# Kernel tuning notes

Hardware: AMD Instinct MI355X
Metric: run time of the kernel (lower is better)

## Reference

```python
import jax, jax.numpy as jnp
import numpy as np

B, QUE, VAL, D = 4, 128, 128, 512

def setup_inputs() -> dict:
    key = jax.random.key(0)
    k = jax.random.split(key, 8)
    return {
        "qs_1": jax.random.normal(k[0], (B, QUE, D), jnp.float32),
        "qs_2": jax.random.normal(k[1], (B, QUE, D), jnp.float32),  # unused by forward, kept for signature fidelity
        "ks":   jax.random.normal(k[2], (B, VAL, D), jnp.float32),
        "vs":   jax.random.normal(k[3], (B, VAL, D), jnp.float32),
        "sg_mask": jax.random.randint(k[4], (B, VAL), 0, 2).astype(bool),  # True = masked
        "W1":  jax.random.normal(k[5], (D, D), jnp.float32) / np.sqrt(D),
        "b1":  jnp.zeros((D,), jnp.float32),
        "Wse": jax.random.normal(k[6], (D, D), jnp.float32) / np.sqrt(D),
        "bse": jnp.zeros((D,), jnp.float32),
        "W2":  jax.random.normal(k[7], (D, 1), jnp.float32) / np.sqrt(D),
        "b2":  jnp.zeros((1,), jnp.float32),
    }

def reference(qs_1, qs_2, ks, vs, sg_mask, W1, b1, Wse, bse, W2, b2):
    # Pairwise query-key elementwise product: [B, que, val, d]
    x = qs_1[:, :, None, :] * ks[:, None, :, :]
    # linear1: Linear(d,d) + ReLU (dropout = identity at eval)
    h = jax.nn.relu(jnp.einsum('bqvd,de->bqve', x, W1) + b1)
    # linear2: Linear(d,1) + ReLU -> scalar score per (q, v) pair
    s = jax.nn.relu(jnp.einsum('bqvd,do->bqvo', h, W2) + b2)[..., 0]  # [B, que, val]
    m = sg_mask[:, None, :]                      # [B, 1, val], True = masked out
    # masked mean of h over the val axis (masked_fill(0) then divide by valid count)
    h = jnp.where(m[..., None], 0.0, h)
    denom = jnp.sum(~sg_mask, axis=-1).astype(h.dtype)      # [B]
    mean = h.sum(axis=2) / denom[:, None, None]             # [B, que, d]
    # squeeze-excitation gate: sigmoid(relu(Linear(d,d)))
    gate = jax.nn.sigmoid(jax.nn.relu(mean @ Wse + bse))    # [B, que, d]
    # masked softmax over val, weighted sum of values
    s = jnp.where(m, -1e9, s)
    w = jax.nn.softmax(s, axis=-1)                          # [B, que, val]
    out = jnp.einsum('bqv,bvd->bqd', w, vs)                 # [B, que, d]
    return gate * out
```

## Files before the change

kernel.cpp:

```cpp
#include <hip/hip_runtime.h>
#include <stdint.h>
#include <stddef.h>

#define BDIM 4
#define QUE  128
#define VAL  128
#define DD   512
#define BQ   (BDIM*QUE)
#define BK   32
#define SROW(r) ((((r) + ((r) >> 2))) & 3)

typedef float    f32x4 __attribute__((ext_vector_type(4)));
typedef float    f32x2 __attribute__((ext_vector_type(2)));
typedef _Float16 f16x8 __attribute__((ext_vector_type(8)));
typedef _Float16 f16x4 __attribute__((ext_vector_type(4)));
typedef _Float16 f16x2 __attribute__((ext_vector_type(2)));

typedef const __attribute__((address_space(1))) void* gas_ptr;
typedef __attribute__((address_space(3))) void*       las_ptr;

__device__ __forceinline__ void async_copy16(const void* g, void* l) {
    __builtin_amdgcn_global_load_lds((gas_ptr)g, (las_ptr)l, 16, 0, 0);
}

__global__ __launch_bounds__(256) void prep_kernel(const float* __restrict__ W1,
                                                   _Float16* __restrict__ W1T,
                                                   const float* __restrict__ Wse,
                                                   _Float16* __restrict__ WseT,
                                                   const float* __restrict__ vs,
                                                   _Float16* __restrict__ vsT) {
    __shared__ float tile[32][33];
    const int tx = threadIdx.x & 31;
    const int ty = threadIdx.x >> 5;
    const int gx = blockIdx.x, gy = blockIdx.y;
    if (gy < 32) {
        const float* src = (gy < 16) ? W1  : Wse;
        _Float16*    dst = (gy < 16) ? W1T : WseT;
        int a0 = gx * 32;
        int b0 = (gy & 15) * 32;
        #pragma unroll
        for (int r = 0; r < 4; ++r)
            tile[ty + r*8][tx] = src[(size_t)(a0 + ty + r*8) * DD + b0 + tx];
        __syncthreads();
        #pragma unroll
        for (int r = 0; r < 4; ++r) {
            int el = ty + r*8;
            dst[(size_t)(b0 + el) * DD + a0 + tx] = (_Float16)tile[tx][el];
        }
    } else {
        int bb = gy - 32;
        const float* src = vs  + (size_t)bb * VAL * DD;
        _Float16*    dst = vsT + (size_t)bb * DD * VAL;
        int b0 = gx * 32;
        for (int vt = 0; vt < 4; ++vt) {
            int a0 = vt * 32;
            __syncthreads();
            #pragma unroll
            for (int r = 0; r < 4; ++r)
                tile[ty + r*8][tx] = src[(size_t)(a0 + ty + r*8) * DD + b0 + tx];
            __syncthreads();
            #pragma unroll
            for (int r = 0; r < 4; ++r) {
                int el = ty + r*8;
                dst[(size_t)(b0 + el) * VAL + a0 + tx] = (_Float16)tile[tx][el];
            }
        }
    }
}

__global__ __launch_bounds__(512, 4) void gemm_h_kernel(
    const float* __restrict__ qs1,
    const float* __restrict__ ks,
    const int*   __restrict__ sgmask,
    const _Float16* __restrict__ W1T,
    const float* __restrict__ b1,
    const float* __restrict__ W2,
    float* __restrict__ s_part,
    float* __restrict__ meansum)
{
    __shared__ _Float16 Ah[128 * BK];
    __shared__ _Float16 Bh[256 * BK];
    __shared__ float qrow[DD];
    __shared__ float sred[4][VAL];
    __shared__ float msumLDS[2][256];

    const int tid  = threadIdx.x;
    const int bq   = blockIdx.x;
    const int gy   = blockIdx.y;
    const int b    = bq >> 7;
    const int lane = tid & 63;
    const int wid  = tid >> 6;
    const int wm   = wid >> 2;
    const int wn   = wid & 3;
    const int quad = lane >> 4;
    const int lr   = lane & 15;

    if (tid < 128)
        *(f32x4*)(qrow + tid * 4) = *(const f32x4*)(qs1 + (size_t)bq * DD + tid * 4);

    f32x4 acc[4][4];
    #pragma unroll
    for (int i = 0; i < 4; ++i)
        #pragma unroll
        for (int j = 0; j < 4; ++j) acc[i][j] = (f32x4){0.f, 0.f, 0.f, 0.f};

    const int r4 = tid >> 2;
    const int cs = tid & 3;
    const int ca = (cs - SROW(r4)) & 3;
    const float* ksrow = ks + ((size_t)b * VAL + r4) * DD + ca * 8;
    const float* qbase = qrow + ca * 8;
    _Float16* a_dst = &Ah[r4 * BK + cs * 8];
    const int rb1 = 128 + r4;
    const int cb1 = (cs - SROW(rb1)) & 3;
    const _Float16* gB0 = W1T + (size_t)(gy * 256 + r4) * DD + ca * 8;
    const _Float16* gB1 = W1T + (size_t)(gy * 256 + rb1) * DD + cb1 * 8;
    _Float16* ldsB0 = &Bh[(wid * 16) * BK];
    _Float16* ldsB1 = &Bh[(128 + wid * 16) * BK];

    const _Float16* fa_ptr[4];
    const _Float16* fb_ptr[4];
    #pragma unroll
    for (int mt = 0; mt < 4; ++mt) {
        int row = wm * 64 + mt * 16 + lr;
        fa_ptr[mt] = &Ah[row * BK + ((quad + SROW(row)) & 3) * 8];
    }
    #pragma unroll
    for (int nt = 0; nt < 4; ++nt) {
        int row = wn * 64 + nt * 16 + lr;
        fb_ptr[nt] = &Bh[row * BK + ((quad + SROW(row)) & 3) * 8];
    }
    __syncthreads();

    for (int kk = 0; kk < DD; kk += BK) {
        async_copy16(gB0 + kk, ldsB0);
        async_copy16(gB1 + kk, ldsB1);
        f32x4 kv0 = *(const f32x4*)(ksrow + kk);
        f32x4 kv1 = *(const f32x4*)(ksrow + kk + 4);
        f32x4 qv0 = *(const f32x4*)(qbase + kk);
        f32x4 qv1 = *(const f32x4*)(qbase + kk + 4);
        f16x8 av;
        #pragma unroll
        for (int c = 0; c < 4; ++c) {
            av[c]     = (_Float16)(kv0[c] * qv0[c]);
            av[c + 4] = (_Float16)(kv1[c] * qv1[c]);
        }
        *(f16x8*)a_dst = av;
        __syncthreads();

        f16x8 fa[4];
        #pragma unroll
        for (int mt = 0; mt < 4; ++mt) fa[mt] = *(const f16x8*)fa_ptr[mt];
        #pragma unroll
        for (int nt = 0; nt < 4; ++nt) {
            f16x8 fb = *(const f16x8*)fb_ptr[nt];
            #pragma unroll
            for (int mt = 0; mt < 4; ++mt)
                acc[mt][nt] = __builtin_amdgcn_mfma_f32_16x16x32_f16(fa[mt], fb, acc[mt][nt], 0, 0, 0);
        }
        __syncthreads();
    }

    float b1v[4], w2v[4];
    #pragma unroll
    for (int nt = 0; nt < 4; ++nt) {
        int col = gy*256 + wn*64 + nt*16 + lr;
        b1v[nt] = b1[col];
        w2v[nt] = W2[col];
    }
    float msum[4] = {0.f, 0.f, 0.f, 0.f};
    #pragma unroll
    for (int mt = 0; mt < 4; ++mt) {
        #pragma unroll
        for (int reg = 0; reg < 4; ++reg) {
            int v = wm*64 + mt*16 + quad*4 + reg;
            int masked = sgmask[b * VAL + v];
            float sacc = 0.f;
            #pragma unroll
            for (int nt = 0; nt < 4; ++nt) {
                float h = acc[mt][nt][reg] + b1v[nt];
                h = fmaxf(h, 0.f);
                sacc += h * w2v[nt];
                if (!masked) msum[nt] += h;
            }
            sacc += __shfl_xor(sacc, 1);
            sacc += __shfl_xor(sacc, 2);
            sacc += __shfl_xor(sacc, 4);
            sacc += __shfl_xor(sacc, 8);
            if (lr == 0) sred[wn][v] = sacc;
        }
    }
    #pragma unroll
    for (int nt = 0; nt < 4; ++nt) {
        float m = msum[nt];
        m += __shfl_xor(m, 16);
        m += __shfl_xor(m, 32);
        if (lane < 16) msumLDS[wm][wn*64 + nt*16 + lr] = m;
    }
    __syncthreads();
    if (tid < 128) {
        s_part[((size_t)bq * 2 + gy) * VAL + tid] =
            sred[0][tid] + sred[1][tid] + sred[2][tid] + sred[3][tid];
    } else if (tid >= 256) {
        int c = tid - 256;
        meansum[(size_t)bq * DD + gy*256 + c] = msumLDS[0][c] + msumLDS[1][c];
    }
}

__global__ __launch_bounds__(64) void mid_kernel(
    const float* __restrict__ s_part,
    const float* __restrict__ meansum,
    const int*   __restrict__ sgmask,
    const float* __restrict__ b2,
    _Float16* __restrict__ wH,
    _Float16* __restrict__ meanH)
{
    const int bq = blockIdx.x;
    const int b  = bq >> 7;
    const int lane = threadIdx.x;
    const float* sp = s_part + (size_t)bq * 2 * VAL;
    float s0 = fmaxf(sp[lane]      + sp[128 + lane]      + b2[0], 0.f);
    float s1 = fmaxf(sp[64 + lane] + sp[192 + lane]      + b2[0], 0.f);
    int m0 = sgmask[b * VAL + lane], m1 = sgmask[b * VAL + 64 + lane];
    float cnt = (m0 ? 0.f : 1.f) + (m1 ? 0.f : 1.f);
    if (m0) s0 = -1e9f;
    if (m1) s1 = -1e9f;
    float mx = fmaxf(s0, s1);
    #pragma unroll
    for (int off = 32; off; off >>= 1) mx = fmaxf(mx, __shfl_xor(mx, off));
    float e0 = __expf(s0 - mx), e1 = __expf(s1 - mx);
    float se = e0 + e1;
    #pragma unroll
    for (int off = 32; off; off >>= 1) {
        se  += __shfl_xor(se, off);
        cnt += __shfl_xor(cnt, off);
    }
    float invse = 1.f / se;
    float invd  = 1.f / cnt;
    f16x2 wv; wv[0] = (_Float16)(e0 * invse); wv[1] = (_Float16)(e1 * invse);
    wH[(size_t)bq * VAL + lane]      = wv[0];
    wH[(size_t)bq * VAL + 64 + lane] = wv[1];
    f32x4 mA = *(const f32x4*)(meansum + (size_t)bq * DD + lane * 8);
    f32x4 mB = *(const f32x4*)(meansum + (size_t)bq * DD + lane * 8 + 4);
    f16x8 mh;
    #pragma unroll
    for (int c = 0; c < 4; ++c) {
        mh[c]     = (_Float16)(mA[c] * invd);
        mh[c + 4] = (_Float16)(mB[c] * invd);
    }
    *(f16x8*)(meanH + (size_t)bq * DD + lane * 8) = mh;
}

__global__ __launch_bounds__(64) void final_kernel(
    const _Float16* __restrict__ meanH,
    const _Float16* __restrict__ WseT,
    const _Float16* __restrict__ wH,
    const _Float16* __restrict__ vsT,
    const float* __restrict__ bse,
    float* __restrict__ out)
{
    const int lane = threadIdx.x;
    const int lr   = lane & 15;
    const int quad = lane >> 4;
    const int q0   = blockIdx.x * 32;
    const int d0   = blockIdx.y * 64;
    const int b    = q0 >> 7;

    f32x4 ga[2][4], oa[2][4];
    #pragma unroll
    for (int i = 0; i < 2; ++i)
        #pragma unroll
        for (int j = 0; j < 4; ++j) { ga[i][j] = (f32x4){0,0,0,0}; oa[i][j] = (f32x4){0,0,0,0}; }

    const _Float16* ap0 = meanH + (size_t)(q0 + lr) * DD + quad * 8;
    const _Float16* bp0 = WseT  + (size_t)(d0 + lr) * DD + quad * 8;
    #pragma unroll 2
    for (int kk = 0; kk < DD; kk += 32) {
        f16x8 am[2];
        #pragma unroll
        for (int mt = 0; mt < 2; ++mt)
            am[mt] = *(const f16x8*)(ap0 + (size_t)mt * 16 * DD + kk);
        #pragma unroll
        for (int nt = 0; nt < 4; ++nt) {
            f16x8 bw = *(const f16x8*)(bp0 + (size_t)nt * 16 * DD + kk);
            #pragma unroll
            for (int mt = 0; mt < 2; ++mt)
                ga[mt][nt] = __builtin_amdgcn_mfma_f32_16x16x32_f16(am[mt], bw, ga[mt][nt], 0, 0, 0);
        }
    }
    const _Float16* wp0 = wH  + (size_t)(q0 + lr) * VAL + quad * 8;
    const _Float16* vp0 = vsT + (size_t)b * DD * VAL + (size_t)(d0 + lr) * VAL + quad * 8;
    #pragma unroll
    for (int kk = 0; kk < VAL; kk += 32) {
        f16x8 am[2];
        #pragma unroll
        for (int mt = 0; mt < 2; ++mt)
            am[mt] = *(const f16x8*)(wp0 + (size_t)mt * 16 * VAL + kk);
        #pragma unroll
        for (int nt = 0; nt < 4; ++nt) {
            f16x8 bv = *(const f16x8*)(vp0 + (size_t)nt * 16 * VAL + kk);
            #pragma unroll
            for (int mt = 0; mt < 2; ++mt)
                oa[mt][nt] = __builtin_amdgcn_mfma_f32_16x16x32_f16(am[mt], bv, oa[mt][nt], 0, 0, 0);
        }
    }
    #pragma unroll
    for (int nt = 0; nt < 4; ++nt) {
        int col = d0 + nt * 16 + lr;
        float bsev = bse[col];
        #pragma unroll
        for (int mt = 0; mt < 2; ++mt) {
            #pragma unroll
            for (int reg = 0; reg < 4; ++reg) {
                int row = q0 + mt * 16 + quad * 4 + reg;
                float garg = ga[mt][nt][reg] + bsev;
                garg = fmaxf(garg, 0.f);
                float gate = 1.f / (1.f + __expf(-garg));
                out[(size_t)row * DD + col] = gate * oa[mt][nt][reg];
            }
        }
    }
}

extern "C" void kernel_launch(void* const* d_in, const int* in_sizes, int n_in,
                              void* d_out, int out_size, void* d_ws, size_t ws_size,
                              hipStream_t stream) {
    (void)in_sizes; (void)n_in; (void)out_size; (void)ws_size;
    const float* qs1 = (const float*)d_in[0];
    const float* ks  = (const float*)d_in[2];
    const float* vs  = (const float*)d_in[3];
    const int*   sg  = (const int*)d_in[4];
    const float* W1  = (const float*)d_in[5];
    const float* b1  = (const float*)d_in[6];
    const float* Wse = (const float*)d_in[7];
    const float* bse = (const float*)d_in[8];
    const float* W2  = (const float*)d_in[9];
    const float* b2  = (const float*)d_in[10];
    float* out = (float*)d_out;

    char* ws = (char*)d_ws;
    _Float16* W1T    = (_Float16*)(ws);
    _Float16* WseT   = (_Float16*)(ws + (512 << 10));
    _Float16* vsT    = (_Float16*)(ws + (1 << 20));
    float*    s_part = (float*)(ws + (1536 << 10));
    float*    msum   = (float*)(ws + (2 << 20));
    _Float16* wH     = (_Float16*)(ws + (3 << 20));
    _Float16* meanH  = (_Float16*)(ws + (3 << 20) + (128 << 10));

    prep_kernel<<<dim3(16, 36), 256, 0, stream>>>(W1, W1T, Wse, WseT, vs, vsT);
    gemm_h_kernel<<<dim3(BQ, 2), 512, 0, stream>>>(qs1, ks, sg, W1T, b1, W2, s_part, msum);
    mid_kernel<<<BQ, 64, 0, stream>>>(s_part, msum, sg, b2, wH, meanH);
    final_kernel<<<dim3(16, 8), 64, 0, stream>>>(meanH, WseT, wH, vsT, bse, out);
}
```

Measured before the change: 139.2 us.

## Double-buffer LDS tiles in gemm_h main loop to overlap loads with MFMA

The A (q*k product) and B (W1T) shared-memory tiles become two buffers each. The next K-slice is loaded into the spare buffer while MFMAs consume the current one, which removes one barrier per iteration. The K loop is now fully unrolled over 16 steps. This doubles the tile LDS footprint, which may cut how many blocks fit per CU below the launch-bounds target. A small cosmetic rewrite of the softmax weight store is also included.

```diff
diff --git a/kernel.cpp b/kernel.cpp
--- a/kernel.cpp
+++ b/kernel.cpp
@@ -78,8 +78,8 @@
     float* __restrict__ s_part,
     float* __restrict__ meansum)
 {
-    __shared__ _Float16 Ah[128 * BK];
-    __shared__ _Float16 Bh[256 * BK];
+    __shared__ _Float16 Ah[2][128 * BK];
+    __shared__ _Float16 Bh[2][256 * BK];
     __shared__ float qrow[DD];
     __shared__ float sred[4][VAL];
     __shared__ float msumLDS[2][256];
@@ -109,50 +109,70 @@
     const int ca = (cs - SROW(r4)) & 3;
     const float* ksrow = ks + ((size_t)b * VAL + r4) * DD + ca * 8;
     const float* qbase = qrow + ca * 8;
-    _Float16* a_dst = &Ah[r4 * BK + cs * 8];
+    const int aoff = r4 * BK + cs * 8;
     const int rb1 = 128 + r4;
     const int cb1 = (cs - SROW(rb1)) & 3;
     const _Float16* gB0 = W1T + (size_t)(gy * 256 + r4) * DD + ca * 8;
     const _Float16* gB1 = W1T + (size_t)(gy * 256 + rb1) * DD + cb1 * 8;
-    _Float16* ldsB0 = &Bh[(wid * 16) * BK];
-    _Float16* ldsB1 = &Bh[(128 + wid * 16) * BK];
-
-    const _Float16* fa_ptr[4];
-    const _Float16* fb_ptr[4];
+    const int boff0 = (wid * 16) * BK;
+    const int boff1 = (128 + wid * 16) * BK;
+
+    int faoff[4], fboff[4];
     #pragma unroll
     for (int mt = 0; mt < 4; ++mt) {
         int row = wm * 64 + mt * 16 + lr;
-        fa_ptr[mt] = &Ah[row * BK + ((quad + SROW(row)) & 3) * 8];
+        faoff[mt] = row * BK + ((quad + SROW(row)) & 3) * 8;
     }
     #pragma unroll
     for (int nt = 0; nt < 4; ++nt) {
         int row = wn * 64 + nt * 16 + lr;
-        fb_ptr[nt] = &Bh[row * BK + ((quad + SROW(row)) & 3) * 8];
+        fboff[nt] = row * BK + ((quad + SROW(row)) & 3) * 8;
     }
     __syncthreads();
 
-    for (int kk = 0; kk < DD; kk += BK) {
-        async_copy16(gB0 + kk, ldsB0);
-        async_copy16(gB1 + kk, ldsB1);
-        f32x4 kv0 = *(const f32x4*)(ksrow + kk);
-        f32x4 kv1 = *(const f32x4*)(ksrow + kk + 4);
-        f32x4 qv0 = *(const f32x4*)(qbase + kk);
-        f32x4 qv1 = *(const f32x4*)(qbase + kk + 4);
+    {
+        async_copy16(gB0, &Bh[0][boff0]);
+        async_copy16(gB1, &Bh[0][boff1]);
+        f32x4 kv0 = *(const f32x4*)(ksrow);
+        f32x4 kv1 = *(const f32x4*)(ksrow + 4);
+        f32x4 qv0 = *(const f32x4*)(qbase);
+        f32x4 qv1 = *(const f32x4*)(qbase + 4);
         f16x8 av;
         #pragma unroll
         for (int c = 0; c < 4; ++c) {
             av[c]     = (_Float16)(kv0[c] * qv0[c]);
             av[c + 4] = (_Float16)(kv1[c] * qv1[c]);
         }
-        *(f16x8*)a_dst = av;
-        __syncthreads();
-
+        *(f16x8*)&Ah[0][aoff] = av;
+    }
+    __syncthreads();
+
+    #pragma unroll
+    for (int i = 0; i < 16; ++i) {
+        const int cur = i & 1;
+        const int nxt = cur ^ 1;
+        if (i < 15) {
+            const int kk = (i + 1) * BK;
+            async_copy16(gB0 + kk, &Bh[nxt][boff0]);
+            async_copy16(gB1 + kk, &Bh[nxt][boff1]);
+            f32x4 kv0 = *(const f32x4*)(ksrow + kk);
+            f32x4 kv1 = *(const f32x4*)(ksrow + kk + 4);
+            f32x4 qv0 = *(const f32x4*)(qbase + kk);
+            f32x4 qv1 = *(const f32x4*)(qbase + kk + 4);
+            f16x8 av;
+            #pragma unroll
+            for (int c = 0; c < 4; ++c) {
+                av[c]     = (_Float16)(kv0[c] * qv0[c]);
+                av[c + 4] = (_Float16)(kv1[c] * qv1[c]);
+            }
+            *(f16x8*)&Ah[nxt][aoff] = av;
+        }
         f16x8 fa[4];
         #pragma unroll
-        for (int mt = 0; mt < 4; ++mt) fa[mt] = *(const f16x8*)fa_ptr[mt];
+        for (int mt = 0; mt < 4; ++mt) fa[mt] = *(const f16x8*)&Ah[cur][faoff[mt]];
         #pragma unroll
         for (int nt = 0; nt < 4; ++nt) {
-            f16x8 fb = *(const f16x8*)fb_ptr[nt];
+            f16x8 fb = *(const f16x8*)&Bh[cur][fboff[nt]];
             #pragma unroll
             for (int mt = 0; mt < 4; ++mt)
                 acc[mt][nt] = __builtin_amdgcn_mfma_f32_16x16x32_f16(fa[mt], fb, acc[mt][nt], 0, 0, 0);
@@ -236,9 +256,8 @@
     }
     float invse = 1.f / se;
     float invd  = 1.f / cnt;
-    f16x2 wv; wv[0] = (_Float16)(e0 * invse); wv[1] = (_Float16)(e1 * invse);
-    wH[(size_t)bq * VAL + lane]      = wv[0];
-    wH[(size_t)bq * VAL + 64 + lane] = wv[1];
+    wH[(size_t)bq * VAL + lane]      = (_Float16)(e0 * invse);
+    wH[(size_t)bq * VAL + 64 + lane] = (_Float16)(e1 * invse);
     f32x4 mA = *(const f32x4*)(meansum + (size_t)bq * DD + lane * 8);
     f32x4 mB = *(const f32x4*)(meansum + (size_t)bq * DD + lane * 8 + 4);
     f16x8 mh;
```

Result: no change. 140.4 us (+0.9%).

## Fuse softmax/mean mid kernel into 1024-thread full-N gemm kernel

Applied to the files above, without the earlier changes.

The h-GEMM kernel now covers all 512 output columns per (b,q) row with 1024 threads (16 waves), where it previously split N across two blocks. With the whole row in one block, the score reduction, masked softmax and mean normalisation that ran in a separate mid kernel move into the epilogue. This drops one launch and the s_part/meansum round trip through global memory. In exchange the grid halves to 512 blocks of 1024 threads with larger LDS use, which may lower occupancy and latency hiding. The A-tile is also recomputed redundantly by fewer threads per element and the epilogue adds extra barriers.

```diff
diff --git a/kernel.cpp b/kernel.cpp
--- a/kernel.cpp
+++ b/kernel.cpp
@@ -68,30 +68,32 @@
     }
 }
 
-__global__ __launch_bounds__(512, 4) void gemm_h_kernel(
+__global__ __launch_bounds__(1024, 4) void gemm_fused_kernel(
     const float* __restrict__ qs1,
     const float* __restrict__ ks,
     const int*   __restrict__ sgmask,
     const _Float16* __restrict__ W1T,
     const float* __restrict__ b1,
     const float* __restrict__ W2,
-    float* __restrict__ s_part,
-    float* __restrict__ meansum)
+    const float* __restrict__ b2,
+    _Float16* __restrict__ wH,
+    _Float16* __restrict__ meanH)
 {
     __shared__ _Float16 Ah[128 * BK];
-    __shared__ _Float16 Bh[256 * BK];
+    __shared__ _Float16 Bh[512 * BK];
     __shared__ float qrow[DD];
-    __shared__ float sred[4][VAL];
-    __shared__ float msumLDS[2][256];
+    __shared__ float sred[8][VAL];
+    __shared__ float msumLDS[2][DD];
+    __shared__ float sv[VAL];
+    __shared__ float redv[2];
 
     const int tid  = threadIdx.x;
     const int bq   = blockIdx.x;
-    const int gy   = blockIdx.y;
     const int b    = bq >> 7;
     const int lane = tid & 63;
     const int wid  = tid >> 6;
-    const int wm   = wid >> 2;
-    const int wn   = wid & 3;
+    const int wm   = wid & 1;
+    const int wn   = wid >> 1;
     const int quad = lane >> 4;
     const int lr   = lane & 15;
 
@@ -104,55 +106,53 @@
         #pragma unroll
         for (int j = 0; j < 4; ++j) acc[i][j] = (f32x4){0.f, 0.f, 0.f, 0.f};
 
-    const int r4 = tid >> 2;
-    const int cs = tid & 3;
-    const int ca = (cs - SROW(r4)) & 3;
-    const float* ksrow = ks + ((size_t)b * VAL + r4) * DD + ca * 8;
-    const float* qbase = qrow + ca * 8;
-    _Float16* a_dst = &Ah[r4 * BK + cs * 8];
-    const int rb1 = 128 + r4;
-    const int cb1 = (cs - SROW(rb1)) & 3;
-    const _Float16* gB0 = W1T + (size_t)(gy * 256 + r4) * DD + ca * 8;
-    const _Float16* gB1 = W1T + (size_t)(gy * 256 + rb1) * DD + cb1 * 8;
+    const int r4  = tid >> 2;
+    const int cs4 = tid & 3;
+    const int cb  = (cs4 - SROW(r4)) & 3;
+    const _Float16* gB0 = W1T + (size_t)r4 * DD + cb * 8;
+    const _Float16* gB1 = W1T + (size_t)(256 + r4) * DD + cb * 8;
     _Float16* ldsB0 = &Bh[(wid * 16) * BK];
-    _Float16* ldsB1 = &Bh[(128 + wid * 16) * BK];
-
-    const _Float16* fa_ptr[4];
-    const _Float16* fb_ptr[4];
+    _Float16* ldsB1 = &Bh[(256 + wid * 16) * BK];
+
+    const int ar  = tid >> 3;
+    const int sub = tid & 7;
+    const int s8  = sub >> 1;
+    const int hf  = sub & 1;
+    const int ca  = (s8 - SROW(ar)) & 3;
+    const float* ksrow = ks + ((size_t)b * VAL + ar) * DD + ca * 8 + hf * 4;
+    const float* qb    = qrow + ca * 8 + hf * 4;
+    const int aoff = ar * BK + s8 * 8 + hf * 4;
+
+    int faoff[4], fboff[4];
     #pragma unroll
     for (int mt = 0; mt < 4; ++mt) {
         int row = wm * 64 + mt * 16 + lr;
-        fa_ptr[mt] = &Ah[row * BK + ((quad + SROW(row)) & 3) * 8];
+        faoff[mt] = row * BK + ((quad + SROW(row)) & 3) * 8;
     }
     #pragma unroll
     for (int nt = 0; nt < 4; ++nt) {
         int row = wn * 64 + nt * 16 + lr;
-        fb_ptr[nt] = &Bh[row * BK + ((quad + SROW(row)) & 3) * 8];
+        fboff[nt] = row * BK + ((quad + SROW(row)) & 3) * 8;
     }
     __syncthreads();
 
     for (int kk = 0; kk < DD; kk += BK) {
         async_copy16(gB0 + kk, ldsB0);
         async_copy16(gB1 + kk, ldsB1);
-        f32x4 kv0 = *(const f32x4*)(ksrow + kk);
-        f32x4 kv1 = *(const f32x4*)(ksrow + kk + 4);
-        f32x4 qv0 = *(const f32x4*)(qbase + kk);
-        f32x4 qv1 = *(const f32x4*)(qbase + kk + 4);
-        f16x8 av;
-        #pragma unroll
-        for (int c = 0; c < 4; ++c) {
-            av[c]     = (_Float16)(kv0[c] * qv0[c]);
-            av[c + 4] = (_Float16)(kv1[c] * qv1[c]);
-        }
-        *(f16x8*)a_dst = av;
+        f32x4 kv = *(const f32x4*)(ksrow + kk);
+        f32x4 qv = *(const f32x4*)(qb + kk);
+        f16x4 av;
+        #pragma unroll
+        for (int c = 0; c < 4; ++c) av[c] = (_Float16)(kv[c] * qv[c]);
+        *(f16x4*)&Ah[aoff] = av;
         __syncthreads();
 
         f16x8 fa[4];
         #pragma unroll
-        for (int mt = 0; mt < 4; ++mt) fa[mt] = *(const f16x8*)fa_ptr[mt];
+        for (int mt = 0; mt < 4; ++mt) fa[mt] = *(const f16x8*)&Ah[faoff[mt]];
         #pragma unroll
         for (int nt = 0; nt < 4; ++nt) {
-            f16x8 fb = *(const f16x8*)fb_ptr[nt];
+            f16x8 fb = *(const f16x8*)&Bh[fboff[nt]];
             #pragma unroll
             for (int mt = 0; mt < 4; ++mt)
                 acc[mt][nt] = __builtin_amdgcn_mfma_f32_16x16x32_f16(fa[mt], fb, acc[mt][nt], 0, 0, 0);
@@ -163,7 +163,7 @@
     float b1v[4], w2v[4];
     #pragma unroll
     for (int nt = 0; nt < 4; ++nt) {
-        int col = gy*256 + wn*64 + nt*16 + lr;
+        int col = wn*64 + nt*16 + lr;
         b1v[nt] = b1[col];
         w2v[nt] = W2[col];
     }
@@ -197,57 +197,43 @@
         if (lane < 16) msumLDS[wm][wn*64 + nt*16 + lr] = m;
     }
     __syncthreads();
+
     if (tid < 128) {
-        s_part[((size_t)bq * 2 + gy) * VAL + tid] =
-            sred[0][tid] + sred[1][tid] + sred[2][tid] + sred[3][tid];
-    } else if (tid >= 256) {
-        int c = tid - 256;
-        meansum[(size_t)bq * DD + gy*256 + c] = msumLDS[0][c] + msumLDS[1][c];
-    }
-}
-
-__global__ __launch_bounds__(64) void mid_kernel(
-    const float* __restrict__ s_part,
-    const float* __restrict__ meansum,
-    const int*   __restrict__ sgmask,
-    const float* __restrict__ b2,
-    _Float16* __restrict__ wH,
-    _Float16* __restrict__ meanH)
-{
-    const int bq = blockIdx.x;
-    const int b  = bq >> 7;
-    const int lane = threadIdx.x;
-    const float* sp = s_part + (size_t)bq * 2 * VAL;
-    float s0 = fmaxf(sp[lane]      + sp[128 + lane]      + b2[0], 0.f);
-    float s1 = fmaxf(sp[64 + lane] + sp[192 + lane]      + b2[0], 0.f);
-    int m0 = sgmask[b * VAL + lane], m1 = sgmask[b * VAL + 64 + lane];
-    float cnt = (m0 ? 0.f : 1.f) + (m1 ? 0.f : 1.f);
-    if (m0) s0 = -1e9f;
-    if (m1) s1 = -1e9f;
-    float mx = fmaxf(s0, s1);
-    #pragma unroll
-    for (int off = 32; off; off >>= 1) mx = fmaxf(mx, __shfl_xor(mx, off));
-    float e0 = __expf(s0 - mx), e1 = __expf(s1 - mx);
-    float se = e0 + e1;
-    #pragma unroll
-    for (int off = 32; off; off >>= 1) {
-        se  += __shfl_xor(se, off);
-        cnt += __shfl_xor(cnt, off);
-    }
-    float invse = 1.f / se;
-    float invd  = 1.f / cnt;
-    f16x2 wv; wv[0] = (_Float16)(e0 * invse); wv[1] = (_Float16)(e1 * invse);
-    wH[(size_t)bq * VAL + lane]      = wv[0];
-    wH[(size_t)bq * VAL + 64 + lane] = wv[1];
-    f32x4 mA = *(const f32x4*)(meansum + (size_t)bq * DD + lane * 8);
-    f32x4 mB = *(const f32x4*)(meansum + (size_t)bq * DD + lane * 8 + 4);
-    f16x8 mh;
-    #pragma unroll
-    for (int c = 0; c < 4; ++c) {
-        mh[c]     = (_Float16)(mA[c] * invd);
-        mh[c + 4] = (_Float16)(mB[c] * invd);
-    }
-    *(f16x8*)(meanH + (size_t)bq * DD + lane * 8) = mh;
+        float ssum = b2[0];
+        #pragma unroll
+        for (int w = 0; w < 8; ++w) ssum += sred[w][tid];
+        ssum = fmaxf(ssum, 0.f);
+        if (sgmask[b * VAL + tid]) ssum = -1e9f;
+        sv[tid] = ssum;
+    }
+    __syncthreads();
+
+    if (tid < 64) {
+        float s0 = sv[tid], s1 = sv[64 + tid];
+        int m0 = sgmask[b * VAL + tid], m1 = sgmask[b * VAL + 64 + tid];
+        float cnt = (m0 ? 0.f : 1.f) + (m1 ? 0.f : 1.f);
+        float mx = fmaxf(s0, s1);
+        #pragma unroll
+        for (int off = 32; off; off >>= 1) mx = fmaxf(mx, __shfl_xor(mx, off));
+        float e0 = __expf(s0 - mx), e1 = __expf(s1 - mx);
+        float se = e0 + e1;
+        #pragma unroll
+        for (int off = 32; off; off >>= 1) {
+            se  += __shfl_xor(se, off);
+            cnt += __shfl_xor(cnt, off);
+        }
+        float invse = 1.f / se;
+        wH[(size_t)bq * VAL + tid]      = (_Float16)(e0 * invse);
+        wH[(size_t)bq * VAL + 64 + tid] = (_Float16)(e1 * invse);
+        if (tid == 0) redv[0] = 1.f / cnt;
+    }
+    __syncthreads();
+
+    if (tid >= 512) {
+        int e = tid - 512;
+        meanH[(size_t)bq * DD + e] =
+            (_Float16)((msumLDS[0][e] + msumLDS[1][e]) * redv[0]);
+    }
 }
 
 __global__ __launch_bounds__(64) void final_kernel(
@@ -338,16 +324,13 @@
     float* out = (float*)d_out;
 
     char* ws = (char*)d_ws;
-    _Float16* W1T    = (_Float16*)(ws);
-    _Float16* WseT   = (_Float16*)(ws + (512 << 10));
-    _Float16* vsT    = (_Float16*)(ws + (1 << 20));
-    float*    s_part = (float*)(ws + (1536 << 10));
-    float*    msum   = (float*)(ws + (2 << 20));
-    _Float16* wH     = (_Float16*)(ws + (3 << 20));
-    _Float16* meanH  = (_Float16*)(ws + (3 << 20) + (128 << 10));
+    _Float16* W1T   = (_Float16*)(ws);
+    _Float16* WseT  = (_Float16*)(ws + (512 << 10));
+    _Float16* vsT   = (_Float16*)(ws + (1 << 20));
+    _Float16* wH    = (_Float16*)(ws + (1536 << 10));
+    _Float16* meanH = (_Float16*)(ws + (1536 << 10) + (128 << 10));
 
     prep_kernel<<<dim3(16, 36), 256, 0, stream>>>(W1, W1T, Wse, WseT, vs, vsT);
-    gemm_h_kernel<<<dim3(BQ, 2), 512, 0, stream>>>(qs1, ks, sg, W1T, b1, W2, s_part, msum);
-    mid_kernel<<<BQ, 64, 0, stream>>>(s_part, msum, sg, b2, wH, meanH);
+    gemm_fused_kernel<<<BQ, 1024, 0, stream>>>(qs1, ks, sg, W1T, b1, W2, b2, wH, meanH);
     final_kernel<<<dim3(16, 8), 64, 0, stream>>>(meanH, WseT, wH, vsT, bse, out);
 }
```

Result: slower. 148.3 us (+6.5%).

## Load MFMA fragments directly from global memory, drop LDS staging in GEMM

Applied to the files above, without the earlier changes.

The gemm_h kernel no longer stages the q*k product tile and W1T tile through shared memory with async copies and barriers. Each lane now loads its own ks rows and W1T rows from global memory, forms the fp16 A fragment in registers, and the K loop is fully unrolled with no __syncthreads. This removes LDS traffic and barrier stalls, but each element is reloaded by the four waves that share it, raising global/L2 traffic and register pressure.

```diff
diff --git a/kernel.cpp b/kernel.cpp
--- a/kernel.cpp
+++ b/kernel.cpp
@@ -8,20 +8,12 @@
 #define DD   512
 #define BQ   (BDIM*QUE)
 #define BK   32
-#define SROW(r) ((((r) + ((r) >> 2))) & 3)
 
 typedef float    f32x4 __attribute__((ext_vector_type(4)));
 typedef float    f32x2 __attribute__((ext_vector_type(2)));
 typedef _Float16 f16x8 __attribute__((ext_vector_type(8)));
 typedef _Float16 f16x4 __attribute__((ext_vector_type(4)));
 typedef _Float16 f16x2 __attribute__((ext_vector_type(2)));
-
-typedef const __attribute__((address_space(1))) void* gas_ptr;
-typedef __attribute__((address_space(3))) void*       las_ptr;
-
-__device__ __forceinline__ void async_copy16(const void* g, void* l) {
-    __builtin_amdgcn_global_load_lds((gas_ptr)g, (las_ptr)l, 16, 0, 0);
-}
 
 __global__ __launch_bounds__(256) void prep_kernel(const float* __restrict__ W1,
                                                    _Float16* __restrict__ W1T,
@@ -78,8 +70,6 @@
     float* __restrict__ s_part,
     float* __restrict__ meansum)
 {
-    __shared__ _Float16 Ah[128 * BK];
-    __shared__ _Float16 Bh[256 * BK];
     __shared__ float qrow[DD];
     __shared__ float sred[4][VAL];
     __shared__ float msumLDS[2][256];
@@ -104,60 +94,39 @@
         #pragma unroll
         for (int j = 0; j < 4; ++j) acc[i][j] = (f32x4){0.f, 0.f, 0.f, 0.f};
 
-    const int r4 = tid >> 2;
-    const int cs = tid & 3;
-    const int ca = (cs - SROW(r4)) & 3;
-    const float* ksrow = ks + ((size_t)b * VAL + r4) * DD + ca * 8;
-    const float* qbase = qrow + ca * 8;
-    _Float16* a_dst = &Ah[r4 * BK + cs * 8];
-    const int rb1 = 128 + r4;
-    const int cb1 = (cs - SROW(rb1)) & 3;
-    const _Float16* gB0 = W1T + (size_t)(gy * 256 + r4) * DD + ca * 8;
-    const _Float16* gB1 = W1T + (size_t)(gy * 256 + rb1) * DD + cb1 * 8;
-    _Float16* ldsB0 = &Bh[(wid * 16) * BK];
-    _Float16* ldsB1 = &Bh[(128 + wid * 16) * BK];
-
-    const _Float16* fa_ptr[4];
-    const _Float16* fb_ptr[4];
-    #pragma unroll
-    for (int mt = 0; mt < 4; ++mt) {
-        int row = wm * 64 + mt * 16 + lr;
-        fa_ptr[mt] = &Ah[row * BK + ((quad + SROW(row)) & 3) * 8];
-    }
-    #pragma unroll
-    for (int nt = 0; nt < 4; ++nt) {
-        int row = wn * 64 + nt * 16 + lr;
-        fb_ptr[nt] = &Bh[row * BK + ((quad + SROW(row)) & 3) * 8];
-    }
+    const float* kbase[4];
+    #pragma unroll
+    for (int mt = 0; mt < 4; ++mt)
+        kbase[mt] = ks + ((size_t)b * VAL + wm*64 + mt*16 + lr) * DD + quad * 8;
+    const _Float16* wbase[4];
+    #pragma unroll
+    for (int nt = 0; nt < 4; ++nt)
+        wbase[nt] = W1T + (size_t)(gy*256 + wn*64 + nt*16 + lr) * DD + quad * 8;
+    const float* qb = qrow + quad * 8;
     __syncthreads();
 
+    #pragma unroll
     for (int kk = 0; kk < DD; kk += BK) {
-        async_copy16(gB0 + kk, ldsB0);
-        async_copy16(gB1 + kk, ldsB1);
-        f32x4 kv0 = *(const f32x4*)(ksrow + kk);
-        f32x4 kv1 = *(const f32x4*)(ksrow + kk + 4);
-        f32x4 qv0 = *(const f32x4*)(qbase + kk);
-        f32x4 qv1 = *(const f32x4*)(qbase + kk + 4);
-        f16x8 av;
-        #pragma unroll
-        for (int c = 0; c < 4; ++c) {
-            av[c]     = (_Float16)(kv0[c] * qv0[c]);
-            av[c + 4] = (_Float16)(kv1[c] * qv1[c]);
-        }
-        *(f16x8*)a_dst = av;
-        __syncthreads();
-
+        f32x4 qv0 = *(const f32x4*)(qb + kk);
+        f32x4 qv1 = *(const f32x4*)(qb + kk + 4);
         f16x8 fa[4];
         #pragma unroll
-        for (int mt = 0; mt < 4; ++mt) fa[mt] = *(const f16x8*)fa_ptr[mt];
+        for (int mt = 0; mt < 4; ++mt) {
+            f32x4 kv0 = *(const f32x4*)(kbase[mt] + kk);
+            f32x4 kv1 = *(const f32x4*)(kbase[mt] + kk + 4);
+            #pragma unroll
+            for (int c = 0; c < 4; ++c) {
+                fa[mt][c]     = (_Float16)(kv0[c] * qv0[c]);
+                fa[mt][c + 4] = (_Float16)(kv1[c] * qv1[c]);
+            }
+        }
         #pragma unroll
         for (int nt = 0; nt < 4; ++nt) {
-            f16x8 fb = *(const f16x8*)fb_ptr[nt];
+            f16x8 fb = *(const f16x8*)(wbase[nt] + kk);
             #pragma unroll
             for (int mt = 0; mt < 4; ++mt)
                 acc[mt][nt] = __builtin_amdgcn_mfma_f32_16x16x32_f16(fa[mt], fb, acc[mt][nt], 0, 0, 0);
         }
-        __syncthreads();
     }
 
     float b1v[4], w2v[4];
@@ -236,9 +205,8 @@
     }
     float invse = 1.f / se;
     float invd  = 1.f / cnt;
-    f16x2 wv; wv[0] = (_Float16)(e0 * invse); wv[1] = (_Float16)(e1 * invse);
-    wH[(size_t)bq * VAL + lane]      = wv[0];
-    wH[(size_t)bq * VAL + 64 + lane] = wv[1];
+    wH[(size_t)bq * VAL + lane]      = (_Float16)(e0 * invse);
+    wH[(size_t)bq * VAL + 64 + lane] = (_Float16)(e1 * invse);
     f32x4 mA = *(const f32x4*)(meansum + (size_t)bq * DD + lane * 8);
     f32x4 mB = *(const f32x4*)(meansum + (size_t)bq * DD + lane * 8 + 4);
     f16x8 mh;
```

Measured after the change: 271.6 us. +95.1%, slower.
